# Kernel tuning notes

Hardware: AMD Instinct MI355X
Metric: run time of the kernel (lower is better)

## Reference

```python
import jax, jax.numpy as jnp
import numpy as np

DEPTH = 8            # max(code_depth)
CODE_DEPTH = (1, 8)  # (vqgan_depth, vqkd_depth)
N_EMBED = 8192
EMBED_DIM = 64
B, H, W = 32, 32, 32


def setup_inputs() -> dict:
    key = jax.random.key(0)
    kx, kc = jax.random.split(key)
    x = jax.random.normal(kx, (B, EMBED_DIM, H, W), dtype=jnp.float32)
    # 8 codebooks, each (n_embed, embed_dim); torch nn.Embedding init is N(0,1)
    codebooks = jax.random.normal(kc, (DEPTH, N_EMBED, EMBED_DIM), dtype=jnp.float32)
    return {"x": x, "codebooks": codebooks}


def _quantize(x_code, codebooks):
    # x_code: (B, h, w, d) -- already stop-gradient'd (torch clones a detached copy)
    b, h, w, d = x_code.shape
    xf = x_code.reshape(-1, d)  # (N, d)

    def step(carry, cb):
        residual, agg = carry
        # squared L2 distances via ||r||^2 + ||c||^2 - 2 r c^T  (torch addmm)
        r_sq = jnp.sum(residual * residual, axis=1, keepdims=True)      # (N, 1)
        c_sq = jnp.sum(cb * cb, axis=1)[None, :]                         # (1, K)
        dist = r_sq + c_sq - 2.0 * (residual @ cb.T)                     # (N, K)
        code = jnp.argmin(dist, axis=1)                                  # (N,)
        quant = cb[code]                                                 # (N, d)
        d_norm = jnp.mean(jnp.sum(dist * dist, axis=-1))
        residual = residual - quant
        agg = agg + quant
        return (residual, agg), (agg, code, d_norm)

    (_, _), (quants, codes, d_norms) = jax.lax.scan(
        step, (xf, jnp.zeros_like(xf)), codebooks)
    quants = quants.reshape(DEPTH, b, h, w, d)             # cumulative quants
    codes = jnp.transpose(codes.reshape(DEPTH, b, h, w), (1, 2, 3, 0))  # (B,h,w,DEPTH)
    return quants, codes, d_norms


def reference(x, codebooks):
    x_code = jnp.transpose(x, (0, 2, 3, 1))  # b c h w -> b h w c
    quants, codes, d_norms = _quantize(jax.lax.stop_gradient(x_code), codebooks)
    # commitment loss: mean over depth of mean((x - agg_quant.detach())^2)
    commit_loss = jnp.mean((x_code[None] - jax.lax.stop_gradient(quants)) ** 2)
    # straight-through outputs in latent (b c h w) shape
    vqkd = jnp.transpose(quants[CODE_DEPTH[1] - 1], (0, 3, 1, 2))
    vqkd_zq = x + jax.lax.stop_gradient(vqkd - x)
    vqgan = jnp.transpose(quants[CODE_DEPTH[0] - 1], (0, 3, 1, 2))
    vqgan_zq = x + jax.lax.stop_gradient(vqgan - x)
    vqkd_d_norm = d_norms[CODE_DEPTH[1] - 1]
    vqgan_d_norm = d_norms[CODE_DEPTH[0] - 1]
    return (vqgan_zq, vqkd_zq, commit_loss, vqkd_d_norm, vqgan_d_norm, codes)
```

## Files before the change

### kernel.cpp

```cpp
#include <hip/hip_runtime.h>

#define OFF_RES    0u
#define OFF_BH     8388608u
#define OFF_BL     9437184u
#define OFF_CSQD   10485760u
#define OFF_CSQH   11010048u
#define OFF_CODES  11272192u
#define OFF_PM1    11403264u
#define OFF_PM2    12451840u
#define OFF_PI1    13500416u
#define OFF_M0     14680064u
#define OFF_M7     14712832u
#define OFF_DNP    14745600u
#define OFF_PCOM   14749760u
#define OFF_PDN    15274048u

#define TAU 3.0e-3f

typedef __attribute__((ext_vector_type(8))) _Float16 f16x8;
typedef __attribute__((ext_vector_type(4))) float f32x4;

__device__ __forceinline__ f32x4 mfma16(f16x8 a, f16x8 b, f32x4 c) {
  return __builtin_amdgcn_mfma_f32_16x16x32_f16(a, b, c, 0, 0, 0);
}

__global__ __launch_bounds__(256) void srq_transpose_init(
    const float* __restrict__ x, float* __restrict__ resid)
{
  __shared__ float tile[64][65];
  const int b   = blockIdx.x >> 4;
  const int hw0 = (blockIdx.x & 15) << 6;
  const int t = threadIdx.x;
#pragma unroll
  for (int i = 0; i < 16; ++i) {
    int e = i * 256 + t;
    int c = e >> 6, hw = e & 63;
    tile[c][hw] = x[(size_t)b * 65536 + (size_t)c * 1024 + hw0 + hw];
  }
  __syncthreads();
#pragma unroll
  for (int i = 0; i < 16; ++i) {
    int e = i * 256 + t;
    int hw = e >> 6, c = e & 63;
    resid[((size_t)(b * 1024 + hw0 + hw) << 6) + c] = tile[c][hw];
  }
}

__global__ __launch_bounds__(256) void srq_csq(
    const float* __restrict__ cb, double* __restrict__ csqD, float* __restrict__ csqH)
{
  int id = blockIdx.x * 256 + threadIdx.x;
  const float* p = cb + ((size_t)id << 6);
  double s = 0.0;
#pragma unroll 8
  for (int d = 0; d < 64; ++d) { double v = (double)p[d]; s = fma(v, v, s); }
  csqD[id] = s;
  csqH[id] = (float)(-0.5 * s);
}

__global__ __launch_bounds__(256) void srq_bconv(
    const float* __restrict__ cb, _Float16* __restrict__ Bh, _Float16* __restrict__ Bl)
{
  int id0 = (blockIdx.x * 256 + threadIdx.x) * 4;
  float4 v = *(const float4*)(cb + id0);
  const float f[4] = {v.x, v.y, v.z, v.w};
#pragma unroll
  for (int u = 0; u < 4; ++u) {
    _Float16 h = (_Float16)f[u];
    Bh[id0 + u] = h;
    Bl[id0 + u] = (_Float16)((f[u] - (float)h) * 2048.f);
  }
}

__global__ __launch_bounds__(256) void srq_dnpre_partial(
    const float* __restrict__ cb, const double* __restrict__ csqD,
    double* __restrict__ Pm, double* __restrict__ Ps1, double* __restrict__ Ps2)
{
  __shared__ float ch[32][64];
  const int t = threadIdx.x;
  const int b = blockIdx.x;
  const int i = t >> 2;
  const int j0 = (t & 3) << 4;
  double acc[16];
#pragma unroll
  for (int n = 0; n < 16; ++n) acc[n] = 0.0;
  double s1 = 0.0, s2 = 0.0;
  for (int c8 = 0; c8 < 8; ++c8) {
    const int kbase = b * 256 + c8 * 32;
    __syncthreads();
    const float* src = cb + (size_t)kbase * 64;
#pragma unroll
    for (int u = 0; u < 2; ++u)
      *(float4*)(&ch[0][0] + (u * 256 + t) * 4) = *(const float4*)(src + (u * 256 + t) * 4);
    __syncthreads();
#pragma unroll 4
    for (int kk = 0; kk < 32; ++kk) {
      double ci = (double)ch[kk][i];
#pragma unroll
      for (int n = 0; n < 16; ++n)
        acc[n] = fma(ci, (double)ch[kk][j0 + n], acc[n]);
    }
    if (t < 64) {
#pragma unroll 4
      for (int kk = 0; kk < 32; ++kk) {
        double v = (double)ch[kk][t];
        s1 += v;
        s2 = fma(csqD[kbase + kk], v, s2);
      }
    }
  }
  double* dst = Pm + ((size_t)b << 12) + (i << 6) + j0;
#pragma unroll
  for (int n = 0; n < 16; ++n) dst[n] = acc[n];
  if (t < 64) { Ps1[(b << 6) + t] = s1; Ps2[(b << 6) + t] = s2; }
}

__global__ __launch_bounds__(256) void srq_dnpre_reduce(
    const double* __restrict__ Pm, const double* __restrict__ Ps1,
    const double* __restrict__ Ps2, const double* __restrict__ csqD,
    double* __restrict__ Mmat, double* __restrict__ S1, double* __restrict__ S2,
    double* __restrict__ CS)
{
  const int t = threadIdx.x;
  if (blockIdx.x < 16) {
    const int e = blockIdx.x * 256 + t;
    double a = 0.0;
    for (int b = 0; b < 32; ++b) a += Pm[((size_t)b << 12) + e];
    Mmat[e] = a;
  } else {
    __shared__ double red[256];
    if (t < 64) {
      double a1 = 0.0, a2 = 0.0;
      for (int b = 0; b < 32; ++b) { a1 += Ps1[(b << 6) + t]; a2 += Ps2[(b << 6) + t]; }
      S1[t] = a1; S2[t] = a2;
    }
    double c1 = 0.0, c2 = 0.0;
    for (int k = t; k < 8192; k += 256) { double q = csqD[k]; c1 += q; c2 = fma(q, q, c2); }
    red[t] = c1;
    __syncthreads();
    for (int o = 128; o; o >>= 1) { if (t < o) red[t] += red[t + o]; __syncthreads(); }
    if (t == 0) CS[0] = red[0];
    __syncthreads();
    red[t] = c2;
    __syncthreads();
    for (int o = 128; o; o >>= 1) { if (t < o) red[t] += red[t + o]; __syncthreads(); }
    if (t == 0) CS[1] = red[0];
  }
}

__device__ __forceinline__ void stage_tile(
    const _Float16* __restrict__ Bh, const _Float16* __restrict__ Bl,
    char* ldsbase, int k0, int wid, int lane)
{
#pragma unroll
  for (int q = 0; q < 4; ++q) {
    int ub = (((q << 2) + wid) << 10);
    int db = ub + lane * 16;
    int half = db >> 13;
    int rowh = (db & 8191) >> 7;
    int soff = (db & 127) ^ ((rowh & 7) << 4);
    const _Float16* g = (half ? Bl : Bh) + (((size_t)(k0 + rowh)) << 6) + (soff >> 1);
    __builtin_amdgcn_global_load_lds(
        (const __attribute__((address_space(1))) void*)g,
        (__attribute__((address_space(3))) void*)(ldsbase + ub), 16, 0, 0);
  }
}

__global__ __launch_bounds__(256, 3) void srq_screen_mfma(
    const _Float16* __restrict__ Bh, const _Float16* __restrict__ Bl,
    const float* __restrict__ csqH, const float* __restrict__ resid,
    float* __restrict__ pm1, float* __restrict__ pm2, int* __restrict__ pi1)
{
  __shared__ char lds[32768];
  const int tid = threadIdx.x;
  const int lane = tid & 63;
  const int wid = tid >> 6;
  const int rg = blockIdx.x & 255;
  const int ks = blockIdx.x >> 8;
  const int k0g = ks << 10;
  const int wrow0 = (rg << 7) + (wid << 5);
  const int lr = lane & 15;
  const int kg = lane >> 4;

  f16x8 ah[2][2], al[2][2];
#pragma unroll
  for (int rf = 0; rf < 2; ++rf)
#pragma unroll
    for (int s = 0; s < 2; ++s) {
      const float* rp = resid + (((size_t)(wrow0 + rf * 16 + lr)) << 6) + s * 32 + kg * 8;
      float4 v0 = *(const float4*)rp;
      float4 v1 = *(const float4*)(rp + 4);
      float f[8] = {v0.x, v0.y, v0.z, v0.w, v1.x, v1.y, v1.z, v1.w};
      f16x8 h, l;
#pragma unroll
      for (int e = 0; e < 8; ++e) {
        _Float16 hh = (_Float16)f[e];
        h[e] = hh;
        l[e] = (_Float16)((f[e] - (float)hh) * 2048.f);
      }
      ah[rf][s] = h;
      al[rf][s] = l;
    }

  float m1[8], m2[8];
  int i1[8];
#pragma unroll
  for (int j = 0; j < 8; ++j) { m1[j] = -3e38f; m2[j] = -3e38f; i1[j] = 0; }

  stage_tile(Bh, Bl, lds, k0g, wid, lane);

  for (int t = 0; t < 16; ++t) {
    __syncthreads();
    if (t < 15) stage_tile(Bh, Bl, lds + (((t + 1) & 1) << 14), k0g + ((t + 1) << 6), wid, lane);
    const char* bb = lds + ((t & 1) << 14);
    const int k0 = k0g + (t << 6);
#pragma unroll
    for (int cf = 0; cf < 4; ++cf) {
      const int cl = cf * 16 + lr;
      const int sw = (cl & 7) << 4;
      const int ro = cl * 128 + kg * 16;
      f16x8 bh0 = *(const f16x8*)(bb + ((ro) ^ sw));
      f16x8 bh1 = *(const f16x8*)(bb + ((ro + 64) ^ sw));
      f16x8 bl0 = *(const f16x8*)(bb + 8192 + ((ro) ^ sw));
      f16x8 bl1 = *(const f16x8*)(bb + 8192 + ((ro + 64) ^ sw));
      const int code = k0 + cl;
      const float ci = csqH[code];
#pragma unroll
      for (int rf = 0; rf < 2; ++rf) {
        f32x4 a1 = {ci, ci, ci, ci};
        f32x4 a2 = {0.f, 0.f, 0.f, 0.f};
        a1 = mfma16(ah[rf][0], bh0, a1);
        a1 = mfma16(ah[rf][1], bh1, a1);
        a2 = mfma16(ah[rf][0], bl0, a2);
        a2 = mfma16(al[rf][0], bh0, a2);
        a2 = mfma16(ah[rf][1], bl1, a2);
        a2 = mfma16(al[rf][1], bh1, a2);
#pragma unroll
        for (int r = 0; r < 4; ++r) {
          float sg = fmaf(4.8828125e-4f, a2[r], a1[r]);
          const int j = rf * 4 + r;
          bool gt = sg > m1[j];
          m2[j] = __builtin_amdgcn_fmed3f(sg, m1[j], m2[j]);
          m1[j] = fmaxf(m1[j], sg);
          i1[j] = gt ? code : i1[j];
        }
      }
    }
  }

#pragma unroll
  for (int j = 0; j < 8; ++j) {
    float a1 = m1[j], a2 = m2[j];
    int ai = i1[j];
#pragma unroll
    for (int w = 1; w <= 8; w <<= 1) {
      float b1 = __shfl_xor(a1, w);
      float b2 = __shfl_xor(a2, w);
      int bi = __shfl_xor(ai, w);
      float nm2 = fmaxf(fminf(a1, b1), fmaxf(a2, b2));
      bool bet = (b1 > a1) || (b1 == a1 && bi < ai);
      a1 = fmaxf(a1, b1);
      ai = bet ? bi : ai;
      a2 = nm2;
    }
    if (lr == 0) {
      const int row = wrow0 + (j >> 2) * 16 + kg * 4 + (j & 3);
      pm1[row * 8 + ks] = -2.f * a1;
      pm2[row * 8 + ks] = -2.f * a2;
      pi1[row * 8 + ks] = ai;
    }
  }
}

template <int NEED_DN>
__global__ __launch_bounds__(256) void srq_merge_update(
    const float* __restrict__ pm1, const float* __restrict__ pm2,
    const int* __restrict__ pi1, const float* __restrict__ cb,
    const double* __restrict__ csqD,
    float* __restrict__ resid, int* __restrict__ codes, float* __restrict__ codesF,
    double* __restrict__ Pcom, double* __restrict__ Pdn,
    const double* __restrict__ Mmat, const double* __restrict__ S1v,
    const double* __restrict__ S2v, const double* __restrict__ CS,
    const float* __restrict__ cbNext, _Float16* __restrict__ BhN,
    _Float16* __restrict__ BlN, int dep)
{
  __shared__ float  rstage[4][64];
  __shared__ double w4[4];
  __shared__ double dnW[4];
  __shared__ int    sflag[4];
  __shared__ int    sbest[4];
  __shared__ double vals[256];
  __shared__ int    idxs[256];
  const int t = threadIdx.x;
  const int team = t >> 6;
  const int c = t & 63;

  if (cbNext) {
    int gid = blockIdx.x * 512 + t;
#pragma unroll
    for (int u = 0; u < 2; ++u) {
      int g2 = gid + u * 256;
      float v = cbNext[g2];
      _Float16 h = (_Float16)v;
      BhN[g2] = h;
      BlN[g2] = (_Float16)((v - (float)h) * 2048.f);
    }
  }

  double comSum = 0.0, dnSum = 0.0;

  for (int g = 0; g < 8; ++g) {
    const int row = (blockIdx.x * 8 + g) * 4 + team;

    float m1 = pm1[row * 8], m2 = pm2[row * 8];
    int i1 = pi1[row * 8];
#pragma unroll
    for (int k = 1; k < 8; ++k) {
      float b1 = pm1[row * 8 + k], b2 = pm2[row * 8 + k];
      int bi = pi1[row * 8 + k];
      m2 = fminf(fmaxf(m1, b1), fminf(m2, b2));
      if (b1 < m1) { m1 = b1; i1 = bi; }
    }
    const bool ok = (m2 - m1) >= TAU;

    const size_t ri = ((size_t)row << 6) + c;
    const float rpre = resid[ri];
    rstage[team][c] = rpre;
    if (c == 0) sflag[team] = ok ? -1 : 1;
    __syncthreads();

    if (NEED_DN) {
      const double rc = (double)rpre;
      double mr = 0.0;
#pragma unroll 4
      for (int i = 0; i < 64; ++i)
        mr = fma(Mmat[i * 64 + c], (double)rstage[team][i], mr);
      double qm = mr * rc;
      double av = rc * S1v[c];
      double b2 = rc * S2v[c];
      double r2 = rc * rc;
#pragma unroll
      for (int o = 32; o; o >>= 1) {
        qm += __shfl_down(qm, o);
        av += __shfl_down(av, o);
        b2 += __shfl_down(b2, o);
        r2 += __shfl_down(r2, o);
      }
      if (c == 0) {
        dnW[team] = 8192.0 * r2 * r2 + CS[1] + 4.0 * qm
                  + 2.0 * r2 * CS[0] - 4.0 * r2 * av - 4.0 * b2;
      }
    }

#pragma unroll 1
    for (int tm = 0; tm < 4; ++tm) {
      if (sflag[tm] != -1) {
        double bv = 1e300;
        int bi = 0x7fffffff;
#pragma unroll 1
        for (int i = 0; i < 32; ++i) {
          int k = i * 256 + t;
          const float* cp = cb + ((size_t)k << 6);
          double a0 = 0.0, a1d = 0.0, a2d = 0.0, a3d = 0.0;
#pragma unroll
          for (int d = 0; d < 64; d += 4) {
            a0  = fma((double)rstage[tm][d    ], (double)cp[d    ], a0);
            a1d = fma((double)rstage[tm][d + 1], (double)cp[d + 1], a1d);
            a2d = fma((double)rstage[tm][d + 2], (double)cp[d + 2], a2d);
            a3d = fma((double)rstage[tm][d + 3], (double)cp[d + 3], a3d);
          }
          double s = csqD[k] - 2.0 * ((a0 + a1d) + (a2d + a3d));
          if (s < bv) { bv = s; bi = k; }
        }
        vals[t] = bv;
        idxs[t] = bi;
        __syncthreads();
        if (t == 0) {
          double gm = vals[0]; int gi = idxs[0];
          for (int u = 1; u < 256; ++u) {
            if (vals[u] < gm || (vals[u] == gm && idxs[u] < gi)) { gm = vals[u]; gi = idxs[u]; }
          }
          sbest[tm] = gi;
        }
        __syncthreads();
      }
    }

    const int codeF = (sflag[team] == -1) ? i1 : sbest[team];
    float q = cb[((size_t)codeF << 6) + c];
    float r = rpre - q;
    resid[ri] = r;
    float p = r * r;
#pragma unroll
    for (int o = 32; o; o >>= 1) p += __shfl_down(p, o);
    if (c == 0) {
      codes[row] = codeF;
      codesF[(size_t)row * 8 + dep] = (float)codeF;
      w4[team] = (double)p;
    }
    __syncthreads();
    if (t == 0) comSum += (w4[0] + w4[1]) + (w4[2] + w4[3]);
    if (NEED_DN && t == 1) dnSum += (dnW[0] + dnW[1]) + (dnW[2] + dnW[3]);
  }

  if (t == 0) Pcom[blockIdx.x] = comSum;
  if (NEED_DN && t == 1) Pdn[blockIdx.x] = dnSum;
}

__global__ __launch_bounds__(256) void srq_writeout(
    const float* __restrict__ x, const float* __restrict__ resid, float* __restrict__ out)
{
  __shared__ float tile[64][65];
  const int b   = blockIdx.x >> 4;
  const int hw0 = (blockIdx.x & 15) << 6;
  const int t = threadIdx.x;
#pragma unroll
  for (int i = 0; i < 16; ++i) {
    int e = i * 256 + t;
    int hw = e >> 6, c = e & 63;
    tile[hw][c] = resid[((size_t)(b * 1024 + hw0 + hw) << 6) + c];
  }
  __syncthreads();
#pragma unroll
  for (int i = 0; i < 16; ++i) {
    int e = i * 256 + t;
    int c = e >> 6, hw = e & 63;
    size_t o = (size_t)b * 65536 + (size_t)c * 1024 + hw0 + hw;
    out[o] = x[o] - tile[hw][c];
  }
}

__global__ __launch_bounds__(256) void srq_finalize(
    const double* __restrict__ Pcom, const double* __restrict__ Pdn,
    float* __restrict__ outs)
{
  __shared__ double red[256];
  const int t = threadIdx.x;
  double s = 0.0;
  for (int i = t; i < 8192; i += 256) s += Pcom[i];
  red[t] = s;
  __syncthreads();
  for (int o = 128; o; o >>= 1) { if (t < o) red[t] += red[t + o]; __syncthreads(); }
  const double commit = red[0];
  __syncthreads();
  s = 0.0;
  for (int i = t; i < 1024; i += 256) s += Pdn[i];
  red[t] = s;
  __syncthreads();
  for (int o = 128; o; o >>= 1) { if (t < o) red[t] += red[t + o]; __syncthreads(); }
  const double dn0 = red[0];
  __syncthreads();
  s = 0.0;
  for (int i = t; i < 1024; i += 256) s += Pdn[1024 + i];
  red[t] = s;
  __syncthreads();
  for (int o = 128; o; o >>= 1) { if (t < o) red[t] += red[t + o]; __syncthreads(); }
  if (t == 0) {
    outs[0] = (float)(commit / 16777216.0);
    outs[1] = (float)(red[0] / 32768.0);
    outs[2] = (float)(dn0 / 32768.0);
  }
}

extern "C" void kernel_launch(void* const* d_in, const int* in_sizes, int n_in,
                              void* d_out, int out_size, void* d_ws, size_t ws_size,
                              hipStream_t stream) {
  const float* x  = (const float*)d_in[0];
  const float* cb = (const float*)d_in[1];
  char* ws = (char*)d_ws;

  float*  resid = (float*)(ws + OFF_RES);
  _Float16* Bh  = (_Float16*)(ws + OFF_BH);
  _Float16* Bl  = (_Float16*)(ws + OFF_BL);
  double* csqD  = (double*)(ws + OFF_CSQD);
  float*  csqH  = (float*)(ws + OFF_CSQH);
  int*    codes = (int*)(ws + OFF_CODES);
  float*  pm1   = (float*)(ws + OFF_PM1);
  float*  pm2   = (float*)(ws + OFF_PM2);
  int*    pi1   = (int*)(ws + OFF_PI1);
  double* M0    = (double*)(ws + OFF_M0);
  double* M7    = (double*)(ws + OFF_M7);
  double* S1_0  = (double*)(ws + OFF_DNP);
  double* S2_0  = (double*)(ws + OFF_DNP + 512);
  double* S1_7  = (double*)(ws + OFF_DNP + 1024);
  double* S2_7  = (double*)(ws + OFF_DNP + 1536);
  double* CS0   = (double*)(ws + OFF_DNP + 2048);
  double* CS7   = (double*)(ws + OFF_DNP + 2064);
  double* Pcom  = (double*)(ws + OFF_PCOM);
  double* Pdn   = (double*)(ws + OFF_PDN);

  double* Pm  = (double*)(ws + OFF_PM1);
  double* Ps1 = (double*)(ws + OFF_PM2);
  double* Ps2 = (double*)(ws + OFF_PI1);

  float* out_vqgan = (float*)d_out;
  float* out_vqkd  = out_vqgan + 2097152;
  float* out_scal  = out_vqgan + 4194304;
  float* out_codes = out_vqgan + 4194307;

  srq_transpose_init<<<512, 256, 0, stream>>>(x, resid);
  srq_csq<<<256, 256, 0, stream>>>(cb, csqD, csqH);
  srq_dnpre_partial<<<32, 256, 0, stream>>>(cb, csqD, Pm, Ps1, Ps2);
  srq_dnpre_reduce<<<17, 256, 0, stream>>>(Pm, Ps1, Ps2, csqD, M0, S1_0, S2_0, CS0);
  srq_dnpre_partial<<<32, 256, 0, stream>>>(cb + (size_t)7 * 524288, csqD + 7 * 8192,
                                            Pm, Ps1, Ps2);
  srq_dnpre_reduce<<<17, 256, 0, stream>>>(Pm, Ps1, Ps2, csqD + 7 * 8192,
                                           M7, S1_7, S2_7, CS7);
  srq_bconv<<<512, 256, 0, stream>>>(cb, Bh, Bl);

  for (int dep = 0; dep < 8; ++dep) {
    const float* cbd = cb + (size_t)dep * 524288;
    const float* cbn = (dep < 7) ? cb + (size_t)(dep + 1) * 524288 : nullptr;
    srq_screen_mfma<<<2048, 256, 0, stream>>>(Bh, Bl, csqH + dep * 8192, resid, pm1, pm2, pi1);
    if (dep == 0 || dep == 7) {
      srq_merge_update<1><<<1024, 256, 0, stream>>>(pm1, pm2, pi1, cbd,
          csqD + dep * 8192, resid, codes, out_codes,
          Pcom + (size_t)dep * 1024, Pdn + (dep == 0 ? 0 : 1024),
          (dep == 0 ? M0 : M7), (dep == 0 ? S1_0 : S1_7),
          (dep == 0 ? S2_0 : S2_7), (dep == 0 ? CS0 : CS7),
          cbn, Bh, Bl, dep);
    } else {
      srq_merge_update<0><<<1024, 256, 0, stream>>>(pm1, pm2, pi1, cbd,
          csqD + dep * 8192, resid, codes, out_codes,
          Pcom + (size_t)dep * 1024, nullptr,
          nullptr, nullptr, nullptr, nullptr,
          cbn, Bh, Bl, dep);
    }
    if (dep == 0) srq_writeout<<<512, 256, 0, stream>>>(x, resid, out_vqgan);
    if (dep == 7) srq_writeout<<<512, 256, 0, stream>>>(x, resid, out_vqkd);
  }
  srq_finalize<<<1, 256, 0, stream>>>(Pcom, Pdn, out_scal);
}
```

Baseline: 2.320 ms.

## Split merge into row-merge, compacted refine list, and separate update kernel

The fused merge/update kernel is split into three kernels. A per-row merge writes the screened code and appends ambiguous rows to a global list via atomics. A refine kernel then runs the exact fp64 search over only the listed rows, and an update kernel applies the residual and loss sums. Previously a whole 4-row block serialized exact searches whenever any of its rows was ambiguous, with several block-wide syncs per group. The change adds two launches per depth, a memset, and an atomic counter, and the order of rows in the list becomes nondeterministic.

```diff
diff --git a/kernel.cpp b/kernel.cpp
--- a/kernel.cpp
+++ b/kernel.cpp
@@ -9,9 +9,11 @@
 #define OFF_PM1    11403264u
 #define OFF_PM2    12451840u
 #define OFF_PI1    13500416u
+#define OFF_FLAG   14548992u
 #define OFF_M0     14680064u
 #define OFF_M7     14712832u
 #define OFF_DNP    14745600u
+#define OFF_FCNT   14749696u
 #define OFF_PCOM   14749760u
 #define OFF_PDN    15274048u
 
@@ -272,25 +274,87 @@
   }
 }
 
+__global__ __launch_bounds__(256) void srq_merge_row(
+    const float* __restrict__ pm1, const float* __restrict__ pm2,
+    const int* __restrict__ pi1, int* __restrict__ codes,
+    int* __restrict__ flagList, int* __restrict__ flagCnt)
+{
+  const int row = blockIdx.x * 256 + threadIdx.x;
+  const float* p1 = pm1 + row * 8;
+  const float* p2 = pm2 + row * 8;
+  const int*   pv = pi1 + row * 8;
+  float m1 = p1[0], m2 = p2[0];
+  int ii = pv[0];
+#pragma unroll
+  for (int k = 1; k < 8; ++k) {
+    float b1 = p1[k], b2 = p2[k];
+    int bi = pv[k];
+    m2 = fminf(fmaxf(m1, b1), fminf(m2, b2));
+    if (b1 < m1) { m1 = b1; ii = bi; }
+  }
+  codes[row] = ii;
+  if (m2 - m1 < TAU) {
+    int pos = atomicAdd(flagCnt, 1);
+    flagList[pos] = row;
+  }
+}
+
+__global__ __launch_bounds__(256) void srq_refine(
+    const float* __restrict__ cb, const double* __restrict__ csqD,
+    const float* __restrict__ resid, int* __restrict__ codes,
+    const int* __restrict__ flagList, const int* __restrict__ flagCnt)
+{
+  __shared__ float rowv[64];
+  __shared__ double vals[256];
+  __shared__ int   idxs[256];
+  int cnt = *flagCnt;
+  for (int j = blockIdx.x; j < cnt; j += gridDim.x) {
+    int row = flagList[j];
+    __syncthreads();
+    if (threadIdx.x < 64) rowv[threadIdx.x] = resid[((size_t)row << 6) + threadIdx.x];
+    __syncthreads();
+    double bv = 1e300;
+    int bi = 0x7fffffff;
+    for (int i = 0; i < 32; ++i) {
+      int k = i * 256 + threadIdx.x;
+      const float* cp = cb + ((size_t)k << 6);
+      double a0 = 0.0, a1 = 0.0, a2 = 0.0, a3 = 0.0;
+#pragma unroll
+      for (int d = 0; d < 64; d += 4) {
+        a0 = fma((double)rowv[d    ], (double)cp[d    ], a0);
+        a1 = fma((double)rowv[d + 1], (double)cp[d + 1], a1);
+        a2 = fma((double)rowv[d + 2], (double)cp[d + 2], a2);
+        a3 = fma((double)rowv[d + 3], (double)cp[d + 3], a3);
+      }
+      double s = csqD[k] - 2.0 * ((a0 + a1) + (a2 + a3));
+      if (s < bv) { bv = s; bi = k; }
+    }
+    vals[threadIdx.x] = bv;
+    idxs[threadIdx.x] = bi;
+    __syncthreads();
+    if (threadIdx.x == 0) {
+      double g = vals[0]; int gi = idxs[0];
+      for (int u = 1; u < 256; ++u) {
+        if (vals[u] < g || (vals[u] == g && idxs[u] < gi)) { g = vals[u]; gi = idxs[u]; }
+      }
+      codes[row] = gi;
+    }
+    __syncthreads();
+  }
+}
+
 template <int NEED_DN>
-__global__ __launch_bounds__(256) void srq_merge_update(
-    const float* __restrict__ pm1, const float* __restrict__ pm2,
-    const int* __restrict__ pi1, const float* __restrict__ cb,
-    const double* __restrict__ csqD,
-    float* __restrict__ resid, int* __restrict__ codes, float* __restrict__ codesF,
+__global__ __launch_bounds__(256) void srq_update(
+    const float* __restrict__ cb, float* __restrict__ resid,
+    const int* __restrict__ codes, float* __restrict__ codesF,
     double* __restrict__ Pcom, double* __restrict__ Pdn,
     const double* __restrict__ Mmat, const double* __restrict__ S1v,
     const double* __restrict__ S2v, const double* __restrict__ CS,
     const float* __restrict__ cbNext, _Float16* __restrict__ BhN,
     _Float16* __restrict__ BlN, int dep)
 {
-  __shared__ float  rstage[4][64];
   __shared__ double w4[4];
-  __shared__ double dnW[4];
-  __shared__ int    sflag[4];
-  __shared__ int    sbest[4];
-  __shared__ double vals[256];
-  __shared__ int    idxs[256];
+  __shared__ double d4[4];
   const int t = threadIdx.x;
   const int team = t >> 6;
   const int c = t & 63;
@@ -307,34 +371,40 @@
     }
   }
 
-  double comSum = 0.0, dnSum = 0.0;
-
+  int rows[8], cds[8];
+#pragma unroll
   for (int g = 0; g < 8; ++g) {
-    const int row = (blockIdx.x * 8 + g) * 4 + team;
-
-    float m1 = pm1[row * 8], m2 = pm2[row * 8];
-    int i1 = pi1[row * 8];
-#pragma unroll
-    for (int k = 1; k < 8; ++k) {
-      float b1 = pm1[row * 8 + k], b2 = pm2[row * 8 + k];
-      int bi = pi1[row * 8 + k];
-      m2 = fminf(fmaxf(m1, b1), fminf(m2, b2));
-      if (b1 < m1) { m1 = b1; i1 = bi; }
-    }
-    const bool ok = (m2 - m1) >= TAU;
-
-    const size_t ri = ((size_t)row << 6) + c;
-    const float rpre = resid[ri];
-    rstage[team][c] = rpre;
-    if (c == 0) sflag[team] = ok ? -1 : 1;
-    __syncthreads();
-
-    if (NEED_DN) {
-      const double rc = (double)rpre;
+    rows[g] = (blockIdx.x * 8 + g) * 4 + team;
+    cds[g] = codes[rows[g]];
+  }
+  float rpre[8], qv[8];
+#pragma unroll
+  for (int g = 0; g < 8; ++g) rpre[g] = resid[((size_t)rows[g] << 6) + c];
+#pragma unroll
+  for (int g = 0; g < 8; ++g) qv[g] = cb[((size_t)cds[g] << 6) + c];
+
+  double com = 0.0, dnSum = 0.0;
+#pragma unroll
+  for (int g = 0; g < 8; ++g) {
+    float r = rpre[g] - qv[g];
+    resid[((size_t)rows[g] << 6) + c] = r;
+    float p = r * r;
+#pragma unroll
+    for (int o = 32; o; o >>= 1) p += __shfl_down(p, o);
+    if (c == 0) {
+      codesF[(size_t)rows[g] * 8 + dep] = (float)cds[g];
+      com += (double)p;
+    }
+  }
+
+  if (NEED_DN) {
+#pragma unroll 1
+    for (int g = 0; g < 8; ++g) {
+      const double rc = (double)rpre[g];
       double mr = 0.0;
 #pragma unroll 4
       for (int i = 0; i < 64; ++i)
-        mr = fma(Mmat[i * 64 + c], (double)rstage[team][i], mr);
+        mr = fma(Mmat[i * 64 + c], (double)__shfl(rpre[g], i), mr);
       double qm = mr * rc;
       double av = rc * S1v[c];
       double b2 = rc * S2v[c];
@@ -346,65 +416,16 @@
         b2 += __shfl_down(b2, o);
         r2 += __shfl_down(r2, o);
       }
-      if (c == 0) {
-        dnW[team] = 8192.0 * r2 * r2 + CS[1] + 4.0 * qm
-                  + 2.0 * r2 * CS[0] - 4.0 * r2 * av - 4.0 * b2;
-      }
-    }
-
-#pragma unroll 1
-    for (int tm = 0; tm < 4; ++tm) {
-      if (sflag[tm] != -1) {
-        double bv = 1e300;
-        int bi = 0x7fffffff;
-#pragma unroll 1
-        for (int i = 0; i < 32; ++i) {
-          int k = i * 256 + t;
-          const float* cp = cb + ((size_t)k << 6);
-          double a0 = 0.0, a1d = 0.0, a2d = 0.0, a3d = 0.0;
-#pragma unroll
-          for (int d = 0; d < 64; d += 4) {
-            a0  = fma((double)rstage[tm][d    ], (double)cp[d    ], a0);
-            a1d = fma((double)rstage[tm][d + 1], (double)cp[d + 1], a1d);
-            a2d = fma((double)rstage[tm][d + 2], (double)cp[d + 2], a2d);
-            a3d = fma((double)rstage[tm][d + 3], (double)cp[d + 3], a3d);
-          }
-          double s = csqD[k] - 2.0 * ((a0 + a1d) + (a2d + a3d));
-          if (s < bv) { bv = s; bi = k; }
-        }
-        vals[t] = bv;
-        idxs[t] = bi;
-        __syncthreads();
-        if (t == 0) {
-          double gm = vals[0]; int gi = idxs[0];
-          for (int u = 1; u < 256; ++u) {
-            if (vals[u] < gm || (vals[u] == gm && idxs[u] < gi)) { gm = vals[u]; gi = idxs[u]; }
-          }
-          sbest[tm] = gi;
-        }
-        __syncthreads();
-      }
-    }
-
-    const int codeF = (sflag[team] == -1) ? i1 : sbest[team];
-    float q = cb[((size_t)codeF << 6) + c];
-    float r = rpre - q;
-    resid[ri] = r;
-    float p = r * r;
-#pragma unroll
-    for (int o = 32; o; o >>= 1) p += __shfl_down(p, o);
-    if (c == 0) {
-      codes[row] = codeF;
-      codesF[(size_t)row * 8 + dep] = (float)codeF;
-      w4[team] = (double)p;
-    }
-    __syncthreads();
-    if (t == 0) comSum += (w4[0] + w4[1]) + (w4[2] + w4[3]);
-    if (NEED_DN && t == 1) dnSum += (dnW[0] + dnW[1]) + (dnW[2] + dnW[3]);
-  }
-
-  if (t == 0) Pcom[blockIdx.x] = comSum;
-  if (NEED_DN && t == 1) Pdn[blockIdx.x] = dnSum;
+      if (c == 0)
+        dnSum += 8192.0 * r2 * r2 + CS[1] + 4.0 * qm
+               + 2.0 * r2 * CS[0] - 4.0 * r2 * av - 4.0 * b2;
+    }
+  }
+
+  if (c == 0) { w4[team] = com; d4[team] = dnSum; }
+  __syncthreads();
+  if (t == 0) Pcom[blockIdx.x] = (w4[0] + w4[1]) + (w4[2] + w4[3]);
+  if (NEED_DN && t == 1) Pdn[blockIdx.x] = (d4[0] + d4[1]) + (d4[2] + d4[3]);
 }
 
 __global__ __launch_bounds__(256) void srq_writeout(
@@ -478,6 +499,7 @@
   float*  pm1   = (float*)(ws + OFF_PM1);
   float*  pm2   = (float*)(ws + OFF_PM2);
   int*    pi1   = (int*)(ws + OFF_PI1);
+  int*    flags = (int*)(ws + OFF_FLAG);
   double* M0    = (double*)(ws + OFF_M0);
   double* M7    = (double*)(ws + OFF_M7);
   double* S1_0  = (double*)(ws + OFF_DNP);
@@ -486,6 +508,7 @@
   double* S2_7  = (double*)(ws + OFF_DNP + 1536);
   double* CS0   = (double*)(ws + OFF_DNP + 2048);
   double* CS7   = (double*)(ws + OFF_DNP + 2064);
+  int*    fcnt  = (int*)(ws + OFF_FCNT);
   double* Pcom  = (double*)(ws + OFF_PCOM);
   double* Pdn   = (double*)(ws + OFF_PDN);
 
@@ -498,6 +521,7 @@
   float* out_scal  = out_vqgan + 4194304;
   float* out_codes = out_vqgan + 4194307;
 
+  hipMemsetAsync(ws + OFF_FCNT, 0, 32, stream);
   srq_transpose_init<<<512, 256, 0, stream>>>(x, resid);
   srq_csq<<<256, 256, 0, stream>>>(cb, csqD, csqH);
   srq_dnpre_partial<<<32, 256, 0, stream>>>(cb, csqD, Pm, Ps1, Ps2);
@@ -512,16 +536,17 @@
     const float* cbd = cb + (size_t)dep * 524288;
     const float* cbn = (dep < 7) ? cb + (size_t)(dep + 1) * 524288 : nullptr;
     srq_screen_mfma<<<2048, 256, 0, stream>>>(Bh, Bl, csqH + dep * 8192, resid, pm1, pm2, pi1);
+    srq_merge_row<<<128, 256, 0, stream>>>(pm1, pm2, pi1, codes, flags, fcnt + dep);
+    srq_refine<<<128, 256, 0, stream>>>(cbd, csqD + dep * 8192, resid, codes,
+                                        flags, fcnt + dep);
     if (dep == 0 || dep == 7) {
-      srq_merge_update<1><<<1024, 256, 0, stream>>>(pm1, pm2, pi1, cbd,
-          csqD + dep * 8192, resid, codes, out_codes,
+      srq_update<1><<<1024, 256, 0, stream>>>(cbd, resid, codes, out_codes,
           Pcom + (size_t)dep * 1024, Pdn + (dep == 0 ? 0 : 1024),
           (dep == 0 ? M0 : M7), (dep == 0 ? S1_0 : S1_7),
           (dep == 0 ? S2_0 : S2_7), (dep == 0 ? CS0 : CS7),
           cbn, Bh, Bl, dep);
     } else {
-      srq_merge_update<0><<<1024, 256, 0, stream>>>(pm1, pm2, pi1, cbd,
-          csqD + dep * 8192, resid, codes, out_codes,
+      srq_update<0><<<1024, 256, 0, stream>>>(cbd, resid, codes, out_codes,
           Pcom + (size_t)dep * 1024, nullptr,
           nullptr, nullptr, nullptr, nullptr,
           cbn, Bh, Bl, dep);
```

Result: faster. 1.856 ms, median of 2 (-20.0%).
